# Performance work log

Hardware: AMD Instinct MI355X
Metric: run time of the kernel (lower is better)

The kernel has to match this reference:

```python
import jax, jax.numpy as jnp
import numpy as np

B, CIN, COUT, KH, KW = 8, 64, 128, 3, 3
H = W = 64
STRIDE, PAD = 1, 1
G = 1  # deformable groups


def setup_inputs() -> dict:
    key = jax.random.key(0)
    k1, k2, k3 = jax.random.split(key, 3)
    rgb = jax.random.normal(k1, (B, CIN, H, W), dtype=jnp.float32)
    # torchvision layout: [B, 2*G*KH*KW, Ho, Wo], (dy, dx) pairs per kernel tap
    offsets = jax.random.normal(k2, (B, 2 * G * KH * KW, H, W), dtype=jnp.float32)
    # xavier_uniform for weight [COUT, CIN, KH, KW]
    fan_in, fan_out = CIN * KH * KW, COUT * KH * KW
    a = float(np.sqrt(6.0 / (fan_in + fan_out)))
    weight = jax.random.uniform(k3, (COUT, CIN, KH, KW), dtype=jnp.float32, minval=-a, maxval=a)
    bias = jnp.zeros((COUT,), dtype=jnp.float32)
    return {"rgb": rgb, "offsets": offsets, "weight": weight, "bias": bias}


def _deform_conv2d(rgb, offsets, weight, bias):
    b, cin, h, w = rgb.shape
    cout, _, kh, kw = weight.shape
    K = kh * kw
    ho = (h + 2 * PAD - kh) // STRIDE + 1
    wo = (w + 2 * PAD - kw) // STRIDE + 1
    cg = cin // G  # channels per deformable group

    off = offsets.reshape(b, G, K, 2, ho, wo)
    dy, dx = off[:, :, :, 0], off[:, :, :, 1]  # [b, G, K, ho, wo]

    ky, kx = jnp.meshgrid(jnp.arange(kh), jnp.arange(kw), indexing="ij")
    ky = ky.reshape(K).astype(jnp.float32)
    kx = kx.reshape(K).astype(jnp.float32)
    base_y = (jnp.arange(ho) * STRIDE - PAD).astype(jnp.float32)
    base_x = (jnp.arange(wo) * STRIDE - PAD).astype(jnp.float32)

    # sampling coordinates: p0 + kernel tap + learned offset -> [b, G, K, ho, wo]
    y = base_y[None, None, None, :, None] + ky[None, None, :, None, None] + dy
    x = base_x[None, None, None, None, :] + kx[None, None, :, None, None] + dx

    y0 = jnp.floor(y)
    x0 = jnp.floor(x)
    fy = y - y0
    fx = x - x0
    y0i = y0.astype(jnp.int32)
    x0i = x0.astype(jnp.int32)

    x_flat = rgb.reshape(b, G, cg, h * w)
    P = K * ho * wo

    def gather_corner(yc, xc, wgt):
        valid = (yc >= 0) & (yc < h) & (xc >= 0) & (xc < w)
        idx = jnp.clip(yc, 0, h - 1) * w + jnp.clip(xc, 0, w - 1)
        wgt = jnp.where(valid, wgt, 0.0).reshape(b, G, 1, P)
        vals = jnp.take_along_axis(x_flat, idx.reshape(b, G, 1, P), axis=3)
        return vals * wgt

    col = (
        gather_corner(y0i, x0i, (1 - fy) * (1 - fx))
        + gather_corner(y0i, x0i + 1, (1 - fy) * fx)
        + gather_corner(y0i + 1, x0i, fy * (1 - fx))
        + gather_corner(y0i + 1, x0i + 1, fy * fx)
    )  # [b, G, cg, K*ho*wo]

    col = col.reshape(b, cin * K, ho * wo)
    out = jnp.einsum("ok,bkp->bop", weight.reshape(cout, cin * K), col)
    return out.reshape(b, cout, ho, wo) + bias[None, :, None, None]


def reference(rgb, offsets, weight, bias):
    return _deform_conv2d(rgb, offsets, weight, bias)
```

## Files before the change

kernel.cpp:

```cpp
#include <hip/hip_runtime.h>

#define B_    8
#define COUT_ 128
#define KP    1024
#define CAPR  16
#define COLST 72
#define COLDW (32 * 36)
#define IMGF  4096

typedef __attribute__((ext_vector_type(8))) __bf16 bf16x8;
typedef unsigned short u16x8 __attribute__((ext_vector_type(8)));
typedef __attribute__((ext_vector_type(4))) float f32x4;

__device__ __forceinline__ unsigned int f2bf(float f) {
    union { float f; unsigned int u; } c; c.f = f;
    unsigned int u = c.u;
    u += 0x7fffu + ((u >> 16) & 1u);
    return u >> 16;
}

__device__ __forceinline__ void gl_lds16(const float* g, float* l) {
    __builtin_amdgcn_global_load_lds(
        (const __attribute__((address_space(1))) unsigned int*)g,
        (__attribute__((address_space(3))) unsigned int*)l, 16, 0, 0);
}

__global__ void prep_weight(const float* __restrict__ w, unsigned short* __restrict__ wbf) {
    int idx = blockIdx.x * 256 + threadIdx.x;
    if (idx >= COUT_ * KP) return;
    int cout = idx >> 10, r = idx & 1023;
    int cinPair = r >> 5, j = r & 31;
    unsigned short v = 0;
    if (j < 18) {
        int k = j >> 1, cinL = j & 1, cin = cinPair * 2 + cinL;
        v = (unsigned short)f2bf(w[(cout * 64 + cin) * 9 + k]);
    }
    wbf[idx] = v;
}

__launch_bounds__(256, 4)
__global__ void deform_mfma3(const float* __restrict__ rgb,
                             const float* __restrict__ off,
                             const unsigned short* __restrict__ wbf,
                             const float* __restrict__ bias,
                             float* __restrict__ out) {
    __shared__ float S[COLDW + 2 * IMGF + 16];
    __shared__ int sYmin, sYmax;
    unsigned int* col32 = (unsigned int*)S;
    unsigned short* col16 = (unsigned short*)S;
    float* imgF = S + COLDW;

    const int t    = threadIdx.x;
    const int bid  = blockIdx.x;
    const int b    = bid & 7;
    const int ho   = (bid >> 3) & 63;
    const int px0  = (bid >> 9) * 32;
    const int px   = t & 31;
    const int tg   = t >> 5;
    const int lane = t & 63;
    const int wv   = t >> 6;
    const int ln15 = lane & 15;
    const int q    = lane >> 4;

    const float* rgbb = rgb + b * (64 * 4096);
    const float* offb = off + b * (2 * 9 * 4096);

    for (int i = t; i < COLDW; i += 256) col32[i] = 0u;
    if (t == 0) { sYmin = 64; sYmax = -1; }
    __syncthreads();

    float m_fy[2], m_fx[2]; int m_y0[2], m_x0[2];
    int lmin = 64, lmax = -1;
#pragma unroll
    for (int ti = 0; ti < 2; ti++) {
        const int kt = ti ? 8 : tg;
        const float dy = offb[((2 * kt)     * 64 + ho) * 64 + px0 + px];
        const float dx = offb[((2 * kt + 1) * 64 + ho) * 64 + px0 + px];
        const float y = (float)(ho - 1 + kt / 3) + dy;
        const float x = (float)(px0 + px - 1 + kt % 3) + dx;
        const float y0f = floorf(y), x0f = floorf(x);
        m_fy[ti] = y - y0f; m_fx[ti] = x - x0f;
        m_y0[ti] = (int)y0f; m_x0[ti] = (int)x0f;
        const int r0 = min(max(m_y0[ti], 0), 63), r1 = min(max(m_y0[ti] + 1, 0), 63);
        lmin = min(lmin, r0); lmax = max(lmax, r1);
    }
    atomicMin(&sYmin, lmin); atomicMax(&sYmax, lmax);
    __syncthreads();
    const int ymin  = sYmin;
    const int nrows = sYmax - ymin + 1;
    const int nr4   = min((nrows + 3) & ~3, CAPR);
    const int ymin2 = max(0, min(ymin, 64 - nr4));

    {
        const float* gb = rgbb + (0 * 4 + wv) * 4096 + ymin2 * 64 + lane * 4;
        float* lb = imgF + wv * (CAPR * 64);
        for (int r4 = 0; r4 < nr4; r4 += 4) gl_lds16(gb + r4 * 64, lb + r4 * 64);
    }

    int mb0[2], mb1[2]; float mw[2][4];
#pragma unroll
    for (int ti = 0; ti < 2; ti++) {
        const int y0 = m_y0[ti], x0 = m_x0[ti];
        const int r0 = min(max(y0, 0), 63) - ymin2;
        const int r1 = min(max(y0 + 1, 0), 63) - ymin2;
        const int roff0 = min(max(r0, 0), CAPR - 1);
        const int roff1 = min(max(r1, 0), CAPR - 1);
        const int xc = min(max(x0, -1), 63);
        mb0[ti] = roff0 * 64 + xc;
        mb1[ti] = roff1 * 64 + xc;
        const float fy = m_fy[ti], fx = m_fx[ti];
        const float vy0 = (y0 >= 0  && y0 < 64) ? 1.f : 0.f;
        const float vy1 = (y0 >= -1 && y0 < 63) ? 1.f : 0.f;
        const float vx0 = (x0 >= 0  && x0 < 64) ? 1.f : 0.f;
        const float vx1 = (x0 >= -1 && x0 < 63) ? 1.f : 0.f;
        const float wy0 = (1.f - fy) * vy0, wy1 = fy * vy1;
        const float wx0 = (1.f - fx) * vx0, wx1 = fx * vx1;
        mw[ti][0] = wy0 * wx0; mw[ti][1] = wy0 * wx1;
        mw[ti][2] = wy1 * wx0; mw[ti][3] = wy1 * wx1;
    }

    f32x4 acc[2][2] = {};
    const unsigned short* wrow0 = wbf + (wv * 32 + ln15) * KP;
    const unsigned short* wrow1 = wrow0 + 16 * KP;

    auto do_unit = [&](int ti, int p, const float* ib, int g) {
        const int kt = ti ? 8 : tg;
        const float* i0 = ib + (2 * p)     * (CAPR * 64);
        const float* i1 = ib + (2 * p + 1) * (CAPR * 64);
        const float w0 = mw[ti][0], w1 = mw[ti][1], w2 = mw[ti][2], w3 = mw[ti][3];
        const int a0 = mb0[ti], a1 = mb1[ti];
        const float ra = w0 * i0[a0] + w1 * i0[a0 + 1] + w2 * i0[a1] + w3 * i0[a1 + 1];
        const float rb = w0 * i1[a0] + w1 * i1[a0 + 1] + w2 * i1[a1] + w3 * i1[a1 + 1];
        col32[px * 36 + p * 16 + kt] = f2bf(ra) | (f2bf(rb) << 16);
        (void)g;
    };

    auto mfma_steps = [&](int gg) {
#pragma unroll
        for (int sg = 0; sg < 2; sg++) {
            const int s = 2 * gg + sg;
            const u16x8 a0u = *(const u16x8*)(wrow0 + s * 32 + q * 8);
            const u16x8 a1u = *(const u16x8*)(wrow1 + s * 32 + q * 8);
            const bf16x8 a0 = __builtin_bit_cast(bf16x8, a0u);
            const bf16x8 a1 = __builtin_bit_cast(bf16x8, a1u);
#pragma unroll
            for (int nj = 0; nj < 2; nj++) {
                const u16x8 bu = *(const u16x8*)(col16 + (nj * 16 + ln15) * COLST + sg * 32 + q * 8);
                const bf16x8 bv = __builtin_bit_cast(bf16x8, bu);
                acc[0][nj] = __builtin_amdgcn_mfma_f32_16x16x32_bf16(a0, bv, acc[0][nj], 0, 0, 0);
                acc[1][nj] = __builtin_amdgcn_mfma_f32_16x16x32_bf16(a1, bv, acc[1][nj], 0, 0, 0);
            }
        }
    };

    __syncthreads();

    for (int g = 0; g < 16; g++) {
        if (g > 0) mfma_steps(g - 1);
        __syncthreads();
        if (g + 1 < 16) {
            const float* gb = rgbb + ((g + 1) * 4 + wv) * 4096 + ymin2 * 64 + lane * 4;
            float* lb = imgF + ((g + 1) & 1) * IMGF + wv * (CAPR * 64);
            for (int r4 = 0; r4 < nr4; r4 += 4) gl_lds16(gb + r4 * 64, lb + r4 * 64);
        }
        {
            const float* ib = imgF + (g & 1) * IMGF;
            do_unit(0, 0, ib, g);
            do_unit(0, 1, ib, g);
            if (tg == (g & 7))       do_unit(1, 0, ib, g);
            if (tg == ((g + 4) & 7)) do_unit(1, 1, ib, g);
        }
        __syncthreads();
    }
    mfma_steps(15);

#pragma unroll
    for (int mi = 0; mi < 2; mi++) {
#pragma unroll
        for (int r = 0; r < 4; r++) {
            const int cout = wv * 32 + mi * 16 + q * 4 + r;
            const float bv = bias[cout];
            float* orow = out + ((b * COUT_ + cout) * 64 + ho) * 64 + px0;
#pragma unroll
            for (int nj = 0; nj < 2; nj++)
                orow[nj * 16 + ln15] = acc[mi][nj][r] + bv;
        }
    }
}

extern "C" void kernel_launch(void* const* d_in, const int* in_sizes, int n_in,
                              void* d_out, int out_size, void* d_ws, size_t ws_size,
                              hipStream_t stream) {
    const float* rgb  = (const float*)d_in[0];
    const float* off  = (const float*)d_in[1];
    const float* w    = (const float*)d_in[2];
    const float* bias = (const float*)d_in[3];
    float* out = (float*)d_out;
    unsigned short* wbf = (unsigned short*)d_ws;

    prep_weight<<<(COUT_ * KP + 255) / 256, 256, 0, stream>>>(w, wbf);
    deform_mfma3<<<1024, 256, 0, stream>>>(rgb, off, wbf, bias, out);
}
```

Before: 116.8 us.

## Prepack RGB as bf16 neighbor pairs and process full rows per block

Adds a prep kernel that converts the input image to bf16 and packs each pixel with its right neighbour into one 32-bit word, so each bilinear row fetch becomes a single LDS load. The main kernel now handles a whole 64-pixel output row per block (512 blocks), double-buffers the column tile, and reorders the weight packing to match 4-channel groups. This is meant to cut LDS gather traffic and halve global image bytes per stage, at the cost of an extra prep pass over the input, bf16 rounding of input pixels, and lower occupancy. A fallback path converts in registers when the workspace is too small.

```diff
diff --git a/kernel.cpp b/kernel.cpp
--- a/kernel.cpp
+++ b/kernel.cpp
@@ -1,12 +1,13 @@
 #include <hip/hip_runtime.h>
 
-#define B_    8
-#define COUT_ 128
-#define KP    1024
-#define CAPR  16
-#define COLST 72
-#define COLDW (32 * 36)
-#define IMGF  4096
+#define COUT_  128
+#define KP     1024
+#define CAPR   20
+#define COLU   36
+#define COLBUF (64 * COLU)
+#define IMGC   (CAPR * 64)
+#define IMGBUF (4 * IMGC)
+#define WS_NEED (size_t)(COUT_ * KP * 2 + 8ull * 64 * 64 * 64 * 4)
 
 typedef __attribute__((ext_vector_type(8))) __bf16 bf16x8;
 typedef unsigned short u16x8 __attribute__((ext_vector_type(8)));
@@ -18,8 +19,10 @@
     u += 0x7fffu + ((u >> 16) & 1u);
     return u >> 16;
 }
-
-__device__ __forceinline__ void gl_lds16(const float* g, float* l) {
+__device__ __forceinline__ float bitsf(unsigned int u) {
+    union { unsigned int u; float f; } c; c.u = u; return c.f;
+}
+__device__ __forceinline__ void gl_lds16(const unsigned int* g, unsigned int* l) {
     __builtin_amdgcn_global_load_lds(
         (const __attribute__((address_space(1))) unsigned int*)g,
         (__attribute__((address_space(3))) unsigned int*)l, 16, 0, 0);
@@ -29,55 +32,60 @@
     int idx = blockIdx.x * 256 + threadIdx.x;
     if (idx >= COUT_ * KP) return;
     int cout = idx >> 10, r = idx & 1023;
-    int cinPair = r >> 5, j = r & 31;
+    int quad = r >> 6, j2 = r & 63;
+    int k = j2 >> 2, j = j2 & 3;
     unsigned short v = 0;
-    if (j < 18) {
-        int k = j >> 1, cinL = j & 1, cin = cinPair * 2 + cinL;
+    if (k < 9) {
+        int cin = quad * 4 + j;
         v = (unsigned short)f2bf(w[(cout * 64 + cin) * 9 + k]);
     }
     wbf[idx] = v;
 }
 
-__launch_bounds__(256, 4)
-__global__ void deform_mfma3(const float* __restrict__ rgb,
+__global__ void prep_rgb(const float* __restrict__ rgb, unsigned int* __restrict__ rgbp) {
+    int idx = blockIdx.x * 256 + threadIdx.x;
+    float a = rgb[idx];
+    float nb = ((idx & 63) == 63) ? 0.f : rgb[idx + 1];
+    rgbp[idx] = f2bf(a) | (f2bf(nb) << 16);
+}
+
+template<bool PREP>
+__launch_bounds__(256, 2)
+__global__ void deform_mfma5(const float* __restrict__ rgb,
+                             const unsigned int* __restrict__ rgbp,
                              const float* __restrict__ off,
                              const unsigned short* __restrict__ wbf,
                              const float* __restrict__ bias,
                              float* __restrict__ out) {
-    __shared__ float S[COLDW + 2 * IMGF + 16];
+    __shared__ unsigned int S[2 * COLBUF + 2 * IMGBUF];
     __shared__ int sYmin, sYmax;
-    unsigned int* col32 = (unsigned int*)S;
-    unsigned short* col16 = (unsigned short*)S;
-    float* imgF = S + COLDW;
+    unsigned int* imgU = S + 2 * COLBUF;
 
     const int t    = threadIdx.x;
     const int bid  = blockIdx.x;
     const int b    = bid & 7;
-    const int ho   = (bid >> 3) & 63;
-    const int px0  = (bid >> 9) * 32;
-    const int px   = t & 31;
-    const int tg   = t >> 5;
+    const int ho   = bid >> 3;
     const int lane = t & 63;
     const int wv   = t >> 6;
+    const int px   = lane;
     const int ln15 = lane & 15;
     const int q    = lane >> 4;
 
-    const float* rgbb = rgb + b * (64 * 4096);
     const float* offb = off + b * (2 * 9 * 4096);
 
-    for (int i = t; i < COLDW; i += 256) col32[i] = 0u;
+    for (int i = t; i < 2 * COLBUF; i += 256) S[i] = 0u;
     if (t == 0) { sYmin = 64; sYmax = -1; }
     __syncthreads();
 
-    float m_fy[2], m_fx[2]; int m_y0[2], m_x0[2];
+    float m_fy[3], m_fx[3]; int m_y0[3], m_x0[3];
     int lmin = 64, lmax = -1;
 #pragma unroll
-    for (int ti = 0; ti < 2; ti++) {
-        const int kt = ti ? 8 : tg;
-        const float dy = offb[((2 * kt)     * 64 + ho) * 64 + px0 + px];
-        const float dx = offb[((2 * kt + 1) * 64 + ho) * 64 + px0 + px];
+    for (int ti = 0; ti < 3; ti++) {
+        const int kt = (ti < 2) ? (wv + ti * 4) : 8;
+        const float dy = offb[((2 * kt)     * 64 + ho) * 64 + px];
+        const float dx = offb[((2 * kt + 1) * 64 + ho) * 64 + px];
         const float y = (float)(ho - 1 + kt / 3) + dy;
-        const float x = (float)(px0 + px - 1 + kt % 3) + dx;
+        const float x = (float)(px - 1 + kt % 3) + dx;
         const float y0f = floorf(y), x0f = floorf(x);
         m_fy[ti] = y - y0f; m_fx[ti] = x - x0f;
         m_y0[ti] = (int)y0f; m_x0[ti] = (int)x0f;
@@ -91,50 +99,80 @@
     const int nr4   = min((nrows + 3) & ~3, CAPR);
     const int ymin2 = max(0, min(ymin, 64 - nr4));
 
-    {
-        const float* gb = rgbb + (0 * 4 + wv) * 4096 + ymin2 * 64 + lane * 4;
-        float* lb = imgF + wv * (CAPR * 64);
-        for (int r4 = 0; r4 < nr4; r4 += 4) gl_lds16(gb + r4 * 64, lb + r4 * 64);
-    }
-
-    int mb0[2], mb1[2]; float mw[2][4];
-#pragma unroll
-    for (int ti = 0; ti < 2; ti++) {
+    float4 sv[5];
+    auto stage_dma = [&](int gg) {
+        const unsigned int* gp = rgbp + ((unsigned)(b * 64 + gg * 4 + wv) * 64 + ymin2) * 64 + lane * 4;
+        unsigned int* lp = imgU + (gg & 1) * IMGBUF + wv * IMGC;
+        for (int r4 = 0; r4 < nr4; r4 += 4) gl_lds16(gp + r4 * 64, lp + r4 * 64);
+    };
+    auto stage_load = [&](int gg) {
+        const float* gp = rgb + ((unsigned)(b * 64 + gg * 4 + wv) * 64 + ymin2 + (lane >> 4)) * 64 + (lane & 15) * 4;
+        int n = 0;
+        for (int r4 = 0; r4 < nr4; r4 += 4, n++) sv[n] = *(const float4*)(gp + r4 * 64);
+    };
+    auto stage_write = [&](int gg) {
+        unsigned int* lp = imgU + (gg & 1) * IMGBUF + wv * IMGC + (lane >> 4) * 64 + (lane & 15) * 4;
+        int n = 0;
+        for (int r4 = 0; r4 < nr4; r4 += 4, n++) {
+            const float4 v = sv[n];
+            unsigned int b0 = f2bf(v.x), b1 = f2bf(v.y), b2 = f2bf(v.z), b3 = f2bf(v.w);
+            unsigned int nb = __shfl(b0, lane + 1);
+            if ((lane & 15) == 15) nb = 0;
+            uint4 pk;
+            pk.x = b0 | (b1 << 16); pk.y = b1 | (b2 << 16);
+            pk.z = b2 | (b3 << 16); pk.w = b3 | (nb << 16);
+            *(uint4*)(lp + r4 * 64) = pk;
+        }
+    };
+
+    int ma0[3], ma1[3]; float mw[3][4];
+#pragma unroll
+    for (int ti = 0; ti < 3; ti++) {
         const int y0 = m_y0[ti], x0 = m_x0[ti];
-        const int r0 = min(max(y0, 0), 63) - ymin2;
-        const int r1 = min(max(y0 + 1, 0), 63) - ymin2;
-        const int roff0 = min(max(r0, 0), CAPR - 1);
-        const int roff1 = min(max(r1, 0), CAPR - 1);
-        const int xc = min(max(x0, -1), 63);
-        mb0[ti] = roff0 * 64 + xc;
-        mb1[ti] = roff1 * 64 + xc;
+        int r0 = min(max(y0, 0), 63) - ymin2;     r0 = min(max(r0, 0), nr4 - 1);
+        int r1 = min(max(y0 + 1, 0), 63) - ymin2; r1 = min(max(r1, 0), nr4 - 1);
+        const int xc = min(max(x0, 0), 63);
+        ma0[ti] = r0 * 64 + xc;
+        ma1[ti] = r1 * 64 + xc;
         const float fy = m_fy[ti], fx = m_fx[ti];
-        const float vy0 = (y0 >= 0  && y0 < 64) ? 1.f : 0.f;
-        const float vy1 = (y0 >= -1 && y0 < 63) ? 1.f : 0.f;
-        const float vx0 = (x0 >= 0  && x0 < 64) ? 1.f : 0.f;
-        const float vx1 = (x0 >= -1 && x0 < 63) ? 1.f : 0.f;
-        const float wy0 = (1.f - fy) * vy0, wy1 = fy * vy1;
-        const float wx0 = (1.f - fx) * vx0, wx1 = fx * vx1;
-        mw[ti][0] = wy0 * wx0; mw[ti][1] = wy0 * wx1;
-        mw[ti][2] = wy1 * wx0; mw[ti][3] = wy1 * wx1;
-    }
-
-    f32x4 acc[2][2] = {};
+        const float wy0 = (y0 >= 0  && y0 < 64) ? (1.f - fy) : 0.f;
+        const float wy1 = (y0 >= -1 && y0 < 63) ? fy         : 0.f;
+        const float wx0 = (x0 >= 0  && x0 < 64) ? (1.f - fx) : 0.f;
+        const float wx1 = (x0 >= -1 && x0 < 63) ? fx         : 0.f;
+        const bool neg = (x0 < 0);
+        const float wA = neg ? wx1 : wx0;
+        const float wB = neg ? 0.f : wx1;
+        mw[ti][0] = wy0 * wA; mw[ti][1] = wy0 * wB;
+        mw[ti][2] = wy1 * wA; mw[ti][3] = wy1 * wB;
+    }
+
+    f32x4 acc[2][4] = {};
     const unsigned short* wrow0 = wbf + (wv * 32 + ln15) * KP;
     const unsigned short* wrow1 = wrow0 + 16 * KP;
-
-    auto do_unit = [&](int ti, int p, const float* ib, int g) {
-        const int kt = ti ? 8 : tg;
-        const float* i0 = ib + (2 * p)     * (CAPR * 64);
-        const float* i1 = ib + (2 * p + 1) * (CAPR * 64);
-        const float w0 = mw[ti][0], w1 = mw[ti][1], w2 = mw[ti][2], w3 = mw[ti][3];
-        const int a0 = mb0[ti], a1 = mb1[ti];
-        const float ra = w0 * i0[a0] + w1 * i0[a0 + 1] + w2 * i0[a1] + w3 * i0[a1 + 1];
-        const float rb = w0 * i1[a0] + w1 * i1[a0 + 1] + w2 * i1[a1] + w3 * i1[a1 + 1];
-        col32[px * 36 + p * 16 + kt] = f2bf(ra) | (f2bf(rb) << 16);
-        (void)g;
-    };
-
+    const unsigned short* col16 = (const unsigned short*)S;
+
+    auto interp1 = [&](const unsigned int* pl, int ti) -> float {
+        const unsigned int tp = pl[ma0[ti]];
+        const unsigned int bp = pl[ma1[ti]];
+        return mw[ti][0] * bitsf(tp << 16) + mw[ti][1] * bitsf(tp & 0xffff0000u)
+             + mw[ti][2] * bitsf(bp << 16) + mw[ti][3] * bitsf(bp & 0xffff0000u);
+    };
+    auto gather = [&](int g) {
+        const unsigned int* ib = imgU + (g & 1) * IMGBUF;
+        unsigned int* cb = S + (g & 1) * COLBUF + px * COLU;
+#pragma unroll
+        for (int ti = 0; ti < 2; ti++) {
+            const int kt = wv + ti * 4;
+            uint2 w2;
+            w2.x = f2bf(interp1(ib, ti))            | (f2bf(interp1(ib + IMGC, ti)) << 16);
+            w2.y = f2bf(interp1(ib + 2 * IMGC, ti)) | (f2bf(interp1(ib + 3 * IMGC, ti)) << 16);
+            *(uint2*)&cb[kt * 2] = w2;
+        }
+        if (wv == (g & 3))
+            cb[16] = f2bf(interp1(ib, 2))            | (f2bf(interp1(ib + IMGC, 2)) << 16);
+        if (wv == ((g + 2) & 3))
+            cb[17] = f2bf(interp1(ib + 2 * IMGC, 2)) | (f2bf(interp1(ib + 3 * IMGC, 2)) << 16);
+    };
     auto mfma_steps = [&](int gg) {
 #pragma unroll
         for (int sg = 0; sg < 2; sg++) {
@@ -144,8 +182,9 @@
             const bf16x8 a0 = __builtin_bit_cast(bf16x8, a0u);
             const bf16x8 a1 = __builtin_bit_cast(bf16x8, a1u);
 #pragma unroll
-            for (int nj = 0; nj < 2; nj++) {
-                const u16x8 bu = *(const u16x8*)(col16 + (nj * 16 + ln15) * COLST + sg * 32 + q * 8);
+            for (int nj = 0; nj < 4; nj++) {
+                const u16x8 bu = *(const u16x8*)(col16 + (gg & 1) * (COLBUF * 2)
+                                                 + (nj * 16 + ln15) * (COLU * 2) + sg * 32 + q * 8);
                 const bf16x8 bv = __builtin_bit_cast(bf16x8, bu);
                 acc[0][nj] = __builtin_amdgcn_mfma_f32_16x16x32_bf16(a0, bv, acc[0][nj], 0, 0, 0);
                 acc[1][nj] = __builtin_amdgcn_mfma_f32_16x16x32_bf16(a1, bv, acc[1][nj], 0, 0, 0);
@@ -153,23 +192,15 @@
         }
     };
 
+    if (PREP) stage_dma(0); else { stage_load(0); }
+    if (!PREP) stage_write(0);
     __syncthreads();
 
     for (int g = 0; g < 16; g++) {
+        if (g + 1 < 16) { if (PREP) stage_dma(g + 1); else stage_load(g + 1); }
         if (g > 0) mfma_steps(g - 1);
-        __syncthreads();
-        if (g + 1 < 16) {
-            const float* gb = rgbb + ((g + 1) * 4 + wv) * 4096 + ymin2 * 64 + lane * 4;
-            float* lb = imgF + ((g + 1) & 1) * IMGF + wv * (CAPR * 64);
-            for (int r4 = 0; r4 < nr4; r4 += 4) gl_lds16(gb + r4 * 64, lb + r4 * 64);
-        }
-        {
-            const float* ib = imgF + (g & 1) * IMGF;
-            do_unit(0, 0, ib, g);
-            do_unit(0, 1, ib, g);
-            if (tg == (g & 7))       do_unit(1, 0, ib, g);
-            if (tg == ((g + 4) & 7)) do_unit(1, 1, ib, g);
-        }
+        gather(g);
+        if (!PREP && g + 1 < 16) stage_write(g + 1);
         __syncthreads();
     }
     mfma_steps(15);
@@ -180,9 +211,9 @@
         for (int r = 0; r < 4; r++) {
             const int cout = wv * 32 + mi * 16 + q * 4 + r;
             const float bv = bias[cout];
-            float* orow = out + ((b * COUT_ + cout) * 64 + ho) * 64 + px0;
-#pragma unroll
-            for (int nj = 0; nj < 2; nj++)
+            float* orow = out + ((b * COUT_ + cout) * 64 + ho) * 64;
+#pragma unroll
+            for (int nj = 0; nj < 4; nj++)
                 orow[nj * 16 + ln15] = acc[mi][nj][r] + bv;
         }
     }
@@ -197,7 +228,13 @@
     const float* bias = (const float*)d_in[3];
     float* out = (float*)d_out;
     unsigned short* wbf = (unsigned short*)d_ws;
+    unsigned int* rgbp  = (unsigned int*)((char*)d_ws + COUT_ * KP * 2);
 
     prep_weight<<<(COUT_ * KP + 255) / 256, 256, 0, stream>>>(w, wbf);
-    deform_mfma3<<<1024, 256, 0, stream>>>(rgb, off, wbf, bias, out);
-}
+    if (ws_size >= WS_NEED) {
+        prep_rgb<<<8 * 64 * 4096 / 256, 256, 0, stream>>>(rgb, rgbp);
+        deform_mfma5<true><<<512, 256, 0, stream>>>(rgb, rgbp, off, wbf, bias, out);
+    } else {
+        deform_mfma5<false><<<512, 256, 0, stream>>>(rgb, nullptr, off, wbf, bias, out);
+    }
+}
```

Measured after the change: 107.8 us. -7.7%, faster.
